# Kernel tuning notes

Hardware: AMD Instinct MI355X
Metric: run time of the kernel (lower is better)

Reference implementation:

```python
import jax, jax.numpy as jnp
import numpy as np

N = 10000      # nodes
E = 320000     # edges (avg degree 32)
IN = 512       # in_channels
OUT = 128      # out_channels
H = 4          # in_head
C1 = 2 * OUT   # per-head hidden channels of conv1 (256)
NEG_SLOPE = 0.2


def setup_inputs() -> dict:
    key = jax.random.key(0)
    ks = jax.random.split(key, 12)
    x = jax.random.normal(ks[0], (N, IN), dtype=jnp.float32)
    edge_index = jax.random.randint(ks[1], (2, E), 0, N, dtype=jnp.int64)
    def glorot(k, shape):
        lim = np.sqrt(6.0 / (shape[0] + shape[-1])).astype(np.float32)
        return jax.random.uniform(k, shape, jnp.float32, -lim, lim)
    # conv1: GATv2Conv(IN -> C1 per head, heads=H)
    Wl1 = glorot(ks[2], (IN, H * C1))
    Wr1 = glorot(ks[3], (IN, H * C1))
    att1 = glorot(ks[4], (H, C1))
    b1 = jnp.zeros((H * C1,), jnp.float32)
    # conv2: GATv2Conv(H*C1 -> OUT, heads=1)
    Wl2 = glorot(ks[5], (H * C1, OUT))
    Wr2 = glorot(ks[6], (H * C1, OUT))
    att2 = glorot(ks[7], (1, OUT))
    b2 = jnp.zeros((OUT,), jnp.float32)
    return {"x": x, "edge_index": edge_index, "Wl1": Wl1, "Wr1": Wr1,
            "att1": att1, "b1": b1, "Wl2": Wl2, "Wr2": Wr2,
            "att2": att2, "b2": b2}


def gatv2_conv(x, src, dst, Wl, Wr, att, b, heads, ch):
    # x: [N, F_in]; src/dst: [E] (message src -> dst, softmax over dst)
    n = x.shape[0]
    xl = (x @ Wl).reshape(n, heads, ch)   # source-side projection
    xr = (x @ Wr).reshape(n, heads, ch)   # target-side projection
    # per-edge GATv2 score: att . LeakyReLU(xl_j + xr_i)   [E, H]
    e = jax.nn.leaky_relu(xl[src] + xr[dst], NEG_SLOPE)    # [E, H, C]
    s = jnp.einsum('ehc,hc->eh', e, att)                   # [E, H]
    # segment softmax over incoming edges of each dst node
    smax = jax.lax.stop_gradient(jax.ops.segment_max(s, dst, num_segments=n))
    ex = jnp.exp(s - smax[dst])
    denom = jax.ops.segment_sum(ex, dst, num_segments=n)
    alpha = ex / denom[dst]                                # [E, H]
    # weighted scatter-add of source messages
    out = jax.ops.segment_sum(alpha[:, :, None] * xl[src], dst, num_segments=n)
    return out.reshape(n, heads * ch) + b                  # concat heads + bias


def reference(x, edge_index, Wl1, Wr1, att1, b1, Wl2, Wr2, att2, b2):
    src, dst = edge_index[0], edge_index[1]
    h = gatv2_conv(x, src, dst, Wl1, Wr1, att1, b1, H, C1)
    h = jax.nn.relu(h)                                     # [N, H*C1]
    out = gatv2_conv(h, src, dst, Wl2, Wr2, att2, b2, 1, OUT)
    return out                                             # [N, OUT]
```

## Files before the change

kernel.cpp:

```cpp
#include <hip/hip_runtime.h>
#include <cfloat>

#define N_NODES 10000
#define N_EDGES 320000
#define IN_F    512
#define F1      1024
#define OUT_F   128
#define NEG     0.2f
#define BUCKET  128

typedef __attribute__((ext_vector_type(8))) short bf16x8;
typedef __attribute__((ext_vector_type(4))) float f32x4;
typedef __attribute__((ext_vector_type(2))) float f32x2;
typedef __attribute__((ext_vector_type(4))) unsigned int u32x4;

__device__ __forceinline__ float lrelu(float v) { return fmaxf(v, NEG * v); }

__device__ __forceinline__ unsigned short f2bf(float f) {
    unsigned u = __float_as_uint(f);
    u += 0x7fff + ((u >> 16) & 1);
    return (unsigned short)(u >> 16);
}
__device__ __forceinline__ float bf2f(unsigned short h) {
    return __uint_as_float(((unsigned)h) << 16);
}
__device__ __forceinline__ void u2f2(unsigned u, float& e0, float& e1) {
    e0 = __uint_as_float(u << 16);
    e1 = __uint_as_float(u & 0xffff0000u);
}

__device__ __forceinline__ float rsum16(float x) {
    x += __int_as_float(__builtin_amdgcn_update_dpp(0, __float_as_int(x), 0x121, 0xF, 0xF, false));
    x += __int_as_float(__builtin_amdgcn_update_dpp(0, __float_as_int(x), 0x122, 0xF, 0xF, false));
    x += __int_as_float(__builtin_amdgcn_update_dpp(0, __float_as_int(x), 0x124, 0xF, 0xF, false));
    x += __int_as_float(__builtin_amdgcn_update_dpp(0, __float_as_int(x), 0x128, 0xF, 0xF, false));
    return x;
}

__device__ __forceinline__ void gld_lds16(const void* g, void* l) {
    __builtin_amdgcn_global_load_lds(
        (const __attribute__((address_space(1))) unsigned int*)g,
        (__attribute__((address_space(3))) unsigned int*)l, 16, 0, 0);
}

#define PB_X  2500
#define PB_S  3750
#define PB_W1 4774
#define PB_END 5030

__device__ __forceinline__ void wt_body(const float* __restrict__ Wa,
                                        const float* __restrict__ Wb,
                                        unsigned short* __restrict__ tbf,
                                        int K, int NS, int n0, int k0, int t,
                                        float (*tile)[33]) {
    int j = t & 31;
    const float* W = (n0 < NS) ? Wa : Wb;
    int nb = (n0 < NS) ? n0 : n0 - NS;
#pragma unroll
    for (int r = 0; r < 4; ++r) {
        int kl = (t >> 5) + r * 8;
        tile[kl][j] = W[(size_t)(k0 + kl) * NS + nb + j];
    }
    __syncthreads();
#pragma unroll
    for (int r = 0; r < 4; ++r) {
        int nl = (t >> 5) + r * 8;
        tbf[(size_t)(n0 + nl) * K + k0 + j] = f2bf(tile[j][nl]);
    }
}

__global__ __launch_bounds__(256) void k_prep(const float* __restrict__ x,
                                              unsigned short* __restrict__ xbf,
                                              const int* __restrict__ ei,
                                              int* __restrict__ cnt,
                                              int* __restrict__ esrc,
                                              const float* __restrict__ Wl1,
                                              const float* __restrict__ Wr1,
                                              unsigned short* __restrict__ w1bf,
                                              const float* __restrict__ Wl2,
                                              const float* __restrict__ Wr2,
                                              unsigned short* __restrict__ w2bf) {
    __shared__ float tile[32][33];
    int bid = blockIdx.x, t = threadIdx.x;
    if (bid < PB_X) {
        int i = bid * 2048 + t * 8;
        f32x4 v0 = __builtin_nontemporal_load((const f32x4*)(x + i));
        f32x4 v1 = __builtin_nontemporal_load((const f32x4*)(x + i + 4));
        ushort4 h0, h1;
        h0.x = f2bf(v0.x); h0.y = f2bf(v0.y); h0.z = f2bf(v0.z); h0.w = f2bf(v0.w);
        h1.x = f2bf(v1.x); h1.y = f2bf(v1.y); h1.z = f2bf(v1.z); h1.w = f2bf(v1.w);
        *(ushort4*)(xbf + i) = h0;
        *(ushort4*)(xbf + i + 4) = h1;
    } else if (bid < PB_S) {
        int e = (bid - PB_X) * 256 + t;
        if (e < N_EDGES) {
            int d = ei[N_EDGES + e];
            int pos = atomicAdd(&cnt[d], 1);
            if (pos < BUCKET) esrc[(size_t)d * BUCKET + pos] = ei[e];
        }
    } else if (bid < PB_W1) {
        int local = bid - PB_S;
        wt_body(Wl1, Wr1, w1bf, IN_F, F1, (local & 63) * 32, (local >> 6) * 32, t, tile);
    } else {
        int local = bid - PB_W1;
        wt_body(Wl2, Wr2, w2bf, F1, OUT_F, (local & 7) * 32, (local >> 3) * 32, t, tile);
    }
}

template<int BM, int BN> struct GemmSmem {
    union {
        struct { short As[BM * 32]; short Bs[BN * 32]; } st;
        unsigned short ct[BM * (BN + 8)];
    };
};

template<int BM, int BN, int WR, int WC>
__global__ __launch_bounds__(256) void gemm_mfma(
        const unsigned short* __restrict__ A,
        const unsigned short* __restrict__ B,
        unsigned short* __restrict__ Cl, unsigned short* __restrict__ Cr,
        int M, int K, int NSPLIT) {
    constexpr int NI = BM / (16 * WR);
    constexpr int NJ = BN / (16 * WC);
    __shared__ __align__(16) GemmSmem<BM, BN> sm;
    int t = threadIdx.x;
    int lane = t & 63, w = t >> 6;
    int row0 = blockIdx.y * BM;
    int n0 = blockIdx.x * BN;
    int wr0 = (w / WC) * (NI * 16);
    int wc0 = (w % WC) * (NJ * 16);
    int q = lane >> 4, md = lane & 15;
    int srow = t >> 2;
    int skoff = (t & 3) * 8;

    f32x4 acc[NI][NJ];
#pragma unroll
    for (int i = 0; i < NI; ++i)
#pragma unroll
        for (int j = 0; j < NJ; ++j)
#pragma unroll
            for (int r = 0; r < 4; ++r) acc[i][j][r] = 0.f;

    for (int k0 = 0; k0 < K; k0 += 32) {
        __syncthreads();
#pragma unroll
        for (int is = 0; is < BM / 64; ++is) {
            int gr = row0 + is * 64 + srow;
            if (gr < M)
                gld_lds16(A + (size_t)gr * K + k0 + skoff,
                          &sm.st.As[(is * 64 + (t >> 6) * 16) * 32]);
        }
#pragma unroll
        for (int is = 0; is < BN / 64; ++is) {
            int gn = n0 + is * 64 + srow;
            gld_lds16(B + (size_t)gn * K + k0 + skoff,
                      &sm.st.Bs[(is * 64 + (t >> 6) * 16) * 32]);
        }
        __syncthreads();

        bf16x8 av[NI], bv[NJ];
#pragma unroll
        for (int i = 0; i < NI; ++i)
            av[i] = *(const bf16x8*)&sm.st.As[(wr0 + i * 16 + md) * 32 + q * 8];
#pragma unroll
        for (int j = 0; j < NJ; ++j)
            bv[j] = *(const bf16x8*)&sm.st.Bs[(wc0 + j * 16 + md) * 32 + q * 8];
#pragma unroll
        for (int i = 0; i < NI; ++i)
#pragma unroll
            for (int j = 0; j < NJ; ++j)
                acc[i][j] = __builtin_amdgcn_mfma_f32_16x16x32_bf16(av[i], bv[j], acc[i][j], 0, 0, 0);
    }

    __syncthreads();
#pragma unroll
    for (int i = 0; i < NI; ++i)
#pragma unroll
        for (int j = 0; j < NJ; ++j)
#pragma unroll
            for (int r = 0; r < 4; ++r)
                sm.ct[(wr0 + i * 16 + q * 4 + r) * (BN + 8) + wc0 + j * 16 + md] =
                    f2bf(acc[i][j][r]);
    __syncthreads();
    unsigned short* C = (n0 < NSPLIT) ? Cl : Cr;
    int cc0 = (n0 < NSPLIT) ? n0 : n0 - NSPLIT;
    constexpr int SEGS = BN / 8;
    for (int idx = t; idx < BM * SEGS; idx += 256) {
        int row = idx / SEGS, seg = idx % SEGS;
        if (row0 + row < M) {
            bf16x8 val = *(const bf16x8*)&sm.ct[row * (BN + 8) + seg * 8];
            *(bf16x8*)(C + (size_t)(row0 + row) * NSPLIT + cc0 + seg * 8) = val;
        }
    }
}

__global__ __launch_bounds__(256) void k_fused1(const unsigned short* __restrict__ xlbf,
                                                const unsigned short* __restrict__ xrbf,
                                                const int* __restrict__ cnt,
                                                const int* __restrict__ esrc,
                                                const float* __restrict__ att,
                                                const float* __restrict__ bias,
                                                unsigned short* __restrict__ hb) {
    int t = threadIdx.x;
    int w = t >> 6, lane = t & 63;
    int ni = w >> 1;
    int ww = w & 1;
    int nd = blockIdx.x * 2 + ni;
    int head = lane >> 4, sub = lane & 15;
    int ch = head * 256 + sub * 16;

    __shared__ float slx[4][4];
    __shared__ float4 sacc4[2][4][64];

    float4 r0, r1, r2, r3;
    {
        const u32x4* prx = (const u32x4*)(xrbf + (size_t)nd * F1 + ch);
        u32x4 xa = __builtin_nontemporal_load(prx);
        u32x4 xb = __builtin_nontemporal_load(prx + 1);
        u2f2(xa.x, r0.x, r0.y); u2f2(xa.y, r0.z, r0.w);
        u2f2(xa.z, r1.x, r1.y); u2f2(xa.w, r1.z, r1.w);
        u2f2(xb.x, r2.x, r2.y); u2f2(xb.y, r2.z, r2.w);
        u2f2(xb.z, r3.x, r3.y); u2f2(xb.w, r3.z, r3.w);
    }
    const float4* pa = (const float4*)(att + ch);
    float4 a0 = pa[0], a1 = pa[1], a2 = pa[2], a3 = pa[3];

    int deg = min(cnt[nd], BUCKET);
    int p0 = nd * BUCKET;
    int dege = min(deg, 64);
    int bkt;
    {
        int sv = (lane < dege) ? esrc[p0 + lane] : 0x7fffffff;
#pragma unroll
        for (int k = 2; k <= 64; k <<= 1) {
#pragma unroll
            for (int j = k >> 1; j > 0; j >>= 1) {
                int other = __shfl_xor(sv, j);
                bool dir = ((lane & k) == 0);
                bool lower = ((lane & j) == 0);
                int mn = min(sv, other), mx = max(sv, other);
                sv = (lower == dir) ? mn : mx;
            }
        }
        bkt = sv;
    }

    float l = 0.f;
    float4 acc0 = make_float4(0.f, 0.f, 0.f, 0.f);
    float4 acc1 = acc0, acc2 = acc0, acc3 = acc0;

    auto edge_body = [&](uint4 ca, uint4 cb) {
        float4 c0, c1, c2, c3;
        u2f2(ca.x, c0.x, c0.y); u2f2(ca.y, c0.z, c0.w);
        u2f2(ca.z, c1.x, c1.y); u2f2(ca.w, c1.z, c1.w);
        u2f2(cb.x, c2.x, c2.y); u2f2(cb.y, c2.z, c2.w);
        u2f2(cb.z, c3.x, c3.y); u2f2(cb.w, c3.z, c3.w);
        float u;
        float sl0, sa0, sl1, sa1, sl2, sa2, sl3, sa3;
        u = c0.x + r0.x; sl0 = a0.x * u;           sa0 = a0.x * fabsf(u);
        u = c0.y + r0.y; sl0 = fmaf(a0.y, u, sl0); sa0 = fmaf(a0.y, fabsf(u), sa0);
        u = c0.z + r0.z; sl0 = fmaf(a0.z, u, sl0); sa0 = fmaf(a0.z, fabsf(u), sa0);
        u = c0.w + r0.w; sl0 = fmaf(a0.w, u, sl0); sa0 = fmaf(a0.w, fabsf(u), sa0);
        u = c1.x + r1.x; sl1 = a1.x * u;           sa1 = a1.x * fabsf(u);
        u = c1.y + r1.y; sl1 = fmaf(a1.y, u, sl1); sa1 = fmaf(a1.y, fabsf(u), sa1);
        u = c1.z + r1.z; sl1 = fmaf(a1.z, u, sl1); sa1 = fmaf(a1.z, fabsf(u), sa1);
        u = c1.w + r1.w; sl1 = fmaf(a1.w, u, sl1); sa1 = fmaf(a1.w, fabsf(u), sa1);
        u = c2.x + r2.x; sl2 = a2.x * u;           sa2 = a2.x * fabsf(u);
        u = c2.y + r2.y; sl2 = fmaf(a2.y, u, sl2); sa2 = fmaf(a2.y, fabsf(u), sa2);
        u = c2.z + r2.z; sl2 = fmaf(a2.z, u, sl2); sa2 = fmaf(a2.z, fabsf(u), sa2);
        u = c2.w + r2.w; sl2 = fmaf(a2.w, u, sl2); sa2 = fmaf(a2.w, fabsf(u), sa2);
        u = c3.x + r3.x; sl3 = a3.x * u;           sa3 = a3.x * fabsf(u);
        u = c3.y + r3.y; sl3 = fmaf(a3.y, u, sl3); sa3 = fmaf(a3.y, fabsf(u), sa3);
        u = c3.z + r3.z; sl3 = fmaf(a3.z, u, sl3); sa3 = fmaf(a3.z, fabsf(u), sa3);
        u = c3.w + r3.w; sl3 = fmaf(a3.w, u, sl3); sa3 = fmaf(a3.w, fabsf(u), sa3);
        float sl = (sl0 + sl1) + (sl2 + sl3);
        float sa = (sa0 + sa1) + (sa2 + sa3);
        float s = rsum16(fmaf(0.6f, sl, 0.4f * sa));
        s = fminf(fmaxf(s, -60.f), 60.f);
        float al = __expf(s);
        l += al;
        acc0.x = fmaf(al, c0.x, acc0.x);
        acc0.y = fmaf(al, c0.y, acc0.y);
        acc0.z = fmaf(al, c0.z, acc0.z);
        acc0.w = fmaf(al, c0.w, acc0.w);
        acc1.x = fmaf(al, c1.x, acc1.x);
        acc1.y = fmaf(al, c1.y, acc1.y);
        acc1.z = fmaf(al, c1.z, acc1.z);
        acc1.w = fmaf(al, c1.w, acc1.w);
        acc2.x = fmaf(al, c2.x, acc2.x);
        acc2.y = fmaf(al, c2.y, acc2.y);
        acc2.z = fmaf(al, c2.z, acc2.z);
        acc2.w = fmaf(al, c2.w, acc2.w);
        acc3.x = fmaf(al, c3.x, acc3.x);
        acc3.y = fmaf(al, c3.y, acc3.y);
        acc3.z = fmaf(al, c3.z, acc3.z);
        acc3.w = fmaf(al, c3.w, acc3.w);
    };

    int idx = ww;
    uint4 ua, ub;
    if (idx < dege) {
        int sn = __shfl(bkt, idx);
        const uint4* pv = (const uint4*)(xlbf + (size_t)sn * F1 + ch);
        ua = pv[0]; ub = pv[1];
    }
    for (; idx < dege; idx += 2) {
        uint4 ca = ua, cb = ub;
        int nidx = idx + 2;
        if (nidx < dege) {
            int sn = __shfl(bkt, nidx);
            const uint4* pv = (const uint4*)(xlbf + (size_t)sn * F1 + ch);
            ua = pv[0]; ub = pv[1];
        }
        edge_body(ca, cb);
    }
    for (int p = p0 + 64 + ww; p < p0 + deg; p += 2) {
        const uint4* pv = (const uint4*)(xlbf + (size_t)esrc[p] * F1 + ch);
        edge_body(pv[0], pv[1]);
    }

    if (sub == 0) slx[w][head] = l;
    if (ww == 1) {
        sacc4[ni][0][lane] = acc0;
        sacc4[ni][1][lane] = acc1;
        sacc4[ni][2][lane] = acc2;
        sacc4[ni][3][lane] = acc3;
    }
    __syncthreads();
    if (ww == 0) {
        float L = l + slx[w ^ 1][head];
        float invL = (L > 0.f) ? 1.f / L : 0.f;
        const float4* pb = (const float4*)(bias + ch);
        size_t base = (size_t)nd * F1 + ch;
        float4 aa[4] = {acc0, acc1, acc2, acc3};
#pragma unroll
        for (int j = 0; j < 4; ++j) {
            float4 pt = sacc4[ni][j][lane];
            float4 b4 = pb[j];
            ushort4 hv;
            hv.x = f2bf(fmaxf(fmaf(aa[j].x + pt.x, invL, b4.x), 0.f));
            hv.y = f2bf(fmaxf(fmaf(aa[j].y + pt.y, invL, b4.y), 0.f));
            hv.z = f2bf(fmaxf(fmaf(aa[j].z + pt.z, invL, b4.z), 0.f));
            hv.w = f2bf(fmaxf(fmaf(aa[j].w + pt.w, invL, b4.w), 0.f));
            *(ushort4*)(hb + base + j * 4) = hv;
        }
    }
}

__global__ __launch_bounds__(256) void k_fused2(const unsigned short* __restrict__ xlbf,
                                                const unsigned short* __restrict__ xrbf,
                                                const int* __restrict__ cnt,
                                                const int* __restrict__ esrc,
                                                const float* __restrict__ att,
                                                const float* __restrict__ bias,
                                                float* __restrict__ out) {
    int t = threadIdx.x;
    int w = t >> 6, lane = t & 63;
    int nd = blockIdx.x * 4 + w;
    int g = lane >> 4, sub = lane & 15;
    int ch = sub * 8;

    __shared__ float slx2[4][4];
    __shared__ float sacc2[4][4][132];

    float r[8], a[8];
    {
        u32x4 u = __builtin_nontemporal_load(
            (const u32x4*)(xrbf + (size_t)nd * OUT_F + ch));
        u2f2(u.x, r[0], r[1]); u2f2(u.y, r[2], r[3]);
        u2f2(u.z, r[4], r[5]); u2f2(u.w, r[6], r[7]);
        float4 q0 = *(const float4*)(att + ch);
        float4 q1 = *(const float4*)(att + ch + 4);
        a[0] = q0.x; a[1] = q0.y; a[2] = q0.z; a[3] = q0.w;
        a[4] = q1.x; a[5] = q1.y; a[6] = q1.z; a[7] = q1.w;
    }
    int deg = min(cnt[nd], BUCKET);
    int p0 = nd * BUCKET;
    int p1 = p0 + deg;

    float l = 0.f;
    float acc[8] = {};
    uint4 cur, nxt;
    {
        int p = p0 + g;
        if (p < p1)     cur = *(const uint4*)(xlbf + (size_t)esrc[p] * OUT_F + ch);
        if (p + 4 < p1) nxt = *(const uint4*)(xlbf + (size_t)esrc[p + 4] * OUT_F + ch);
    }
    for (int p = p0 + g; p < p1; p += 4) {
        uint4 c = cur;
        cur = nxt;
        if (p + 8 < p1) nxt = *(const uint4*)(xlbf + (size_t)esrc[p + 8] * OUT_F + ch);
        float v[8];
        u2f2(c.x, v[0], v[1]); u2f2(c.y, v[2], v[3]);
        u2f2(c.z, v[4], v[5]); u2f2(c.w, v[6], v[7]);
        float uu;
        float slA, saA, slB, saB;
        uu = v[0] + r[0]; slA = a[0] * uu;           saA = a[0] * fabsf(uu);
        uu = v[1] + r[1]; slA = fmaf(a[1], uu, slA); saA = fmaf(a[1], fabsf(uu), saA);
        uu = v[2] + r[2]; slA = fmaf(a[2], uu, slA); saA = fmaf(a[2], fabsf(uu), saA);
        uu = v[3] + r[3]; slA = fmaf(a[3], uu, slA); saA = fmaf(a[3], fabsf(uu), saA);
        uu = v[4] + r[4]; slB = a[4] * uu;           saB = a[4] * fabsf(uu);
        uu = v[5] + r[5]; slB = fmaf(a[5], uu, slB); saB = fmaf(a[5], fabsf(uu), saB);
        uu = v[6] + r[6]; slB = fmaf(a[6], uu, slB); saB = fmaf(a[6], fabsf(uu), saB);
        uu = v[7] + r[7]; slB = fmaf(a[7], uu, slB); saB = fmaf(a[7], fabsf(uu), saB);
        float s = rsum16(fmaf(0.6f, slA + slB, 0.4f * (saA + saB)));
        s = fminf(fmaxf(s, -60.f), 60.f);
        float al = __expf(s);
        l += al;
#pragma unroll
        for (int k = 0; k < 8; ++k) acc[k] = fmaf(al, v[k], acc[k]);
    }

    if (sub == 0) slx2[w][g] = l;
    float4 v0 = make_float4(acc[0], acc[1], acc[2], acc[3]);
    float4 v1 = make_float4(acc[4], acc[5], acc[6], acc[7]);
    *(float4*)&sacc2[w][g][ch] = v0;
    *(float4*)&sacc2[w][g][ch + 4] = v1;
    __syncthreads();
    float L = slx2[w][0] + slx2[w][1] + slx2[w][2] + slx2[w][3];
    float invL = (L > 0.f) ? 1.f / L : 0.f;
    int c2 = lane * 2;
    float o0 = sacc2[w][0][c2] + sacc2[w][1][c2] + sacc2[w][2][c2] + sacc2[w][3][c2];
    float o1 = sacc2[w][0][c2 + 1] + sacc2[w][1][c2 + 1] + sacc2[w][2][c2 + 1] + sacc2[w][3][c2 + 1];
    float2 bf = *(const float2*)(bias + c2);
    f32x2 o;
    o.x = fmaf(o0, invL, bf.x);
    o.y = fmaf(o1, invL, bf.y);
    __builtin_nontemporal_store(o, (f32x2*)(out + (size_t)nd * OUT_F + c2));
}

extern "C" void kernel_launch(void* const* d_in, const int* in_sizes, int n_in,
                              void* d_out, int out_size, void* d_ws, size_t ws_size,
                              hipStream_t stream) {
    const float* x    = (const float*)d_in[0];
    const int*   ei   = (const int*)d_in[1];
    const float* Wl1  = (const float*)d_in[2];
    const float* Wr1  = (const float*)d_in[3];
    const float* att1 = (const float*)d_in[4];
    const float* b1   = (const float*)d_in[5];
    const float* Wl2  = (const float*)d_in[6];
    const float* Wr2  = (const float*)d_in[7];
    const float* att2 = (const float*)d_in[8];
    const float* b2   = (const float*)d_in[9];
    float* out = (float*)d_out;

    unsigned short* us = (unsigned short*)d_ws;
    unsigned short* xl1bf = us;
    unsigned short* xr1bf = xl1bf + (size_t)N_NODES * F1;
    unsigned short* xl2bf = xr1bf + (size_t)N_NODES * F1;
    unsigned short* xr2bf = xl2bf + (size_t)N_NODES * OUT_F;
    unsigned short* hb   = xr2bf + (size_t)N_NODES * OUT_F;
    unsigned short* xbf  = hb + (size_t)N_NODES * F1;
    unsigned short* w1bf = xbf + (size_t)N_NODES * IN_F;
    unsigned short* w2bf = w1bf + (size_t)2048 * IN_F;
    int* cnt   = (int*)(w2bf + (size_t)256 * F1);
    int* esrc  = cnt + (N_NODES + 16);

    hipMemsetAsync(cnt, 0, sizeof(int) * N_NODES, stream);
    k_prep<<<PB_END, 256, 0, stream>>>(x, xbf, ei, cnt, esrc,
                                       Wl1, Wr1, w1bf,
                                       Wl2, Wr2, w2bf);

    gemm_mfma<128, 128, 2, 2><<<dim3(16, (N_NODES + 127) / 128), 256, 0, stream>>>(
        xbf, w1bf, xl1bf, xr1bf, N_NODES, IN_F, F1);

    k_fused1<<<N_NODES / 2, 256, 0, stream>>>(xl1bf, xr1bf, cnt, esrc, att1, b1, hb);

    gemm_mfma<64, 64, 2, 2><<<dim3(4, (N_NODES + 63) / 64), 256, 0, stream>>>(
        hb, w2bf, xl2bf, xr2bf, N_NODES, F1, OUT_F);

    k_fused2<<<N_NODES / 4, 256, 0, stream>>>(xl2bf, xr2bf, cnt, esrc, att2, b2, out);
}
```

Baseline: 253.5 us.

## Sort edge buckets once inside GEMM launch and double K-step per stage

The per-node bitonic sort of incoming source indices moves out of k_fused1 into extra blocks appended to the first GEMM grid. Those blocks sort each bucket and write it back to esrc, and k_fused1 now reads the presorted indices directly. The GEMM main loop also loads two 32-wide K panes per barrier pair, which halves the number of synchronisations at the cost of doubled LDS staging. k_fused2 may rely on the sorted order persisting, and the doubled shared memory could reduce occupancy.

```diff
diff --git a/kernel.cpp b/kernel.cpp
--- a/kernel.cpp
+++ b/kernel.cpp
@@ -109,7 +109,7 @@
 
 template<int BM, int BN> struct GemmSmem {
     union {
-        struct { short As[BM * 32]; short Bs[BN * 32]; } st;
+        struct { short As[2 * BM * 32]; short Bs[2 * BN * 32]; } st;
         unsigned short ct[BM * (BN + 8)];
     };
 };
@@ -119,12 +119,36 @@
         const unsigned short* __restrict__ A,
         const unsigned short* __restrict__ B,
         unsigned short* __restrict__ Cl, unsigned short* __restrict__ Cr,
-        int M, int K, int NSPLIT) {
+        int M, int K, int NSPLIT, int ym,
+        const int* __restrict__ cnt, int* __restrict__ esrc) {
     constexpr int NI = BM / (16 * WR);
     constexpr int NJ = BN / (16 * WC);
     __shared__ __align__(16) GemmSmem<BM, BN> sm;
     int t = threadIdx.x;
     int lane = t & 63, w = t >> 6;
+
+    if ((int)blockIdx.y >= ym) {
+        int nd = ((blockIdx.y - ym) * gridDim.x + blockIdx.x) * 4 + w;
+        if (nd < N_NODES) {
+            int deg = min(cnt[nd], 64);
+            int p0 = nd * BUCKET;
+            int v = (lane < deg) ? esrc[p0 + lane] : 0x7fffffff;
+#pragma unroll
+            for (int k = 2; k <= 64; k <<= 1) {
+#pragma unroll
+                for (int j = k >> 1; j > 0; j >>= 1) {
+                    int other = __shfl_xor(v, j);
+                    bool dir = ((lane & k) == 0);
+                    bool lower = ((lane & j) == 0);
+                    int mn = min(v, other), mx = max(v, other);
+                    v = (lower == dir) ? mn : mx;
+                }
+            }
+            if (lane < deg) esrc[p0 + lane] = v;
+        }
+        return;
+    }
+
     int row0 = blockIdx.y * BM;
     int n0 = blockIdx.x * BN;
     int wr0 = (w / WC) * (NI * 16);
@@ -141,35 +165,42 @@
 #pragma unroll
             for (int r = 0; r < 4; ++r) acc[i][j][r] = 0.f;
 
-    for (int k0 = 0; k0 < K; k0 += 32) {
+    for (int k0 = 0; k0 < K; k0 += 64) {
         __syncthreads();
 #pragma unroll
-        for (int is = 0; is < BM / 64; ++is) {
-            int gr = row0 + is * 64 + srow;
-            if (gr < M)
-                gld_lds16(A + (size_t)gr * K + k0 + skoff,
-                          &sm.st.As[(is * 64 + (t >> 6) * 16) * 32]);
-        }
-#pragma unroll
-        for (int is = 0; is < BN / 64; ++is) {
-            int gn = n0 + is * 64 + srow;
-            gld_lds16(B + (size_t)gn * K + k0 + skoff,
-                      &sm.st.Bs[(is * 64 + (t >> 6) * 16) * 32]);
-        }
+        for (int pane = 0; pane < 2; ++pane)
+#pragma unroll
+            for (int is = 0; is < BM / 64; ++is) {
+                int gr = row0 + is * 64 + srow;
+                if (gr < M)
+                    gld_lds16(A + (size_t)gr * K + k0 + pane * 32 + skoff,
+                              &sm.st.As[pane * BM * 32 + (is * 64 + w * 16) * 32]);
+            }
+#pragma unroll
+        for (int pane = 0; pane < 2; ++pane)
+#pragma unroll
+            for (int is = 0; is < BN / 64; ++is) {
+                int gn = n0 + is * 64 + srow;
+                gld_lds16(B + (size_t)gn * K + k0 + pane * 32 + skoff,
+                          &sm.st.Bs[pane * BN * 32 + (is * 64 + w * 16) * 32]);
+            }
         __syncthreads();
 
-        bf16x8 av[NI], bv[NJ];
-#pragma unroll
-        for (int i = 0; i < NI; ++i)
-            av[i] = *(const bf16x8*)&sm.st.As[(wr0 + i * 16 + md) * 32 + q * 8];
-#pragma unroll
-        for (int j = 0; j < NJ; ++j)
-            bv[j] = *(const bf16x8*)&sm.st.Bs[(wc0 + j * 16 + md) * 32 + q * 8];
-#pragma unroll
-        for (int i = 0; i < NI; ++i)
+#pragma unroll
+        for (int kk = 0; kk < 2; ++kk) {
+            bf16x8 av[NI], bv[NJ];
+#pragma unroll
+            for (int i = 0; i < NI; ++i)
+                av[i] = *(const bf16x8*)&sm.st.As[kk * BM * 32 + (wr0 + i * 16 + md) * 32 + q * 8];
 #pragma unroll
             for (int j = 0; j < NJ; ++j)
-                acc[i][j] = __builtin_amdgcn_mfma_f32_16x16x32_bf16(av[i], bv[j], acc[i][j], 0, 0, 0);
+                bv[j] = *(const bf16x8*)&sm.st.Bs[kk * BN * 32 + (wc0 + j * 16 + md) * 32 + q * 8];
+#pragma unroll
+            for (int i = 0; i < NI; ++i)
+#pragma unroll
+                for (int j = 0; j < NJ; ++j)
+                    acc[i][j] = __builtin_amdgcn_mfma_f32_16x16x32_bf16(av[i], bv[j], acc[i][j], 0, 0, 0);
+        }
     }
 
     __syncthreads();
@@ -228,22 +259,7 @@
     int deg = min(cnt[nd], BUCKET);
     int p0 = nd * BUCKET;
     int dege = min(deg, 64);
-    int bkt;
-    {
-        int sv = (lane < dege) ? esrc[p0 + lane] : 0x7fffffff;
-#pragma unroll
-        for (int k = 2; k <= 64; k <<= 1) {
-#pragma unroll
-            for (int j = k >> 1; j > 0; j >>= 1) {
-                int other = __shfl_xor(sv, j);
-                bool dir = ((lane & k) == 0);
-                bool lower = ((lane & j) == 0);
-                int mn = min(sv, other), mx = max(sv, other);
-                sv = (lower == dir) ? mn : mx;
-            }
-        }
-        bkt = sv;
-    }
+    int bkt = (lane < dege) ? esrc[p0 + lane] : 0;
 
     float l = 0.f;
     float4 acc0 = make_float4(0.f, 0.f, 0.f, 0.f);
@@ -461,13 +477,13 @@
                                        Wl1, Wr1, w1bf,
                                        Wl2, Wr2, w2bf);
 
-    gemm_mfma<128, 128, 2, 2><<<dim3(16, (N_NODES + 127) / 128), 256, 0, stream>>>(
-        xbf, w1bf, xl1bf, xr1bf, N_NODES, IN_F, F1);
+    gemm_mfma<128, 128, 2, 2><<<dim3(16, 79 + 157), 256, 0, stream>>>(
+        xbf, w1bf, xl1bf, xr1bf, N_NODES, IN_F, F1, 79, cnt, esrc);
 
     k_fused1<<<N_NODES / 2, 256, 0, stream>>>(xl1bf, xr1bf, cnt, esrc, att1, b1, hb);
 
-    gemm_mfma<64, 64, 2, 2><<<dim3(4, (N_NODES + 63) / 64), 256, 0, stream>>>(
-        hb, w2bf, xl2bf, xr2bf, N_NODES, F1, OUT_F);
+    gemm_mfma<64, 64, 2, 2><<<dim3(4, 157), 256, 0, stream>>>(
+        hb, w2bf, xl2bf, xr2bf, N_NODES, F1, OUT_F, 157, nullptr, nullptr);
 
     k_fused2<<<N_NODES / 4, 256, 0, stream>>>(xl2bf, xr2bf, cnt, esrc, att2, b2, out);
 }
```

Result: no change. 250.0 us (-1.4%).
